# Kernel tuning notes

Hardware: AMD Instinct MI355X
Metric: run time of the kernel (lower is better)

Reference implementation:

```python
import jax, jax.numpy as jnp
import numpy as np

N_NODES = 100000
N_EDGES = 1200000
D = 64


def setup_inputs() -> dict:
    key = jax.random.key(0)
    ks = jax.random.split(key, 11)
    feats = jax.random.normal(ks[0], (N_NODES, D), dtype=jnp.float32)
    src = jax.random.randint(ks[1], (N_EDGES,), 0, N_NODES)
    dst = jax.random.randint(ks[2], (N_EDGES,), 0, N_NODES)
    s = 0.1  # small init scale
    W1 = jax.random.normal(ks[3], (D, D), dtype=jnp.float32) * s
    b1 = jnp.zeros((D,), dtype=jnp.float32)
    Wr1 = jax.random.normal(ks[4], (D, D), dtype=jnp.float32) * s
    br1 = jnp.zeros((D,), dtype=jnp.float32)
    W2 = jax.random.normal(ks[5], (D, D), dtype=jnp.float32) * s
    b2 = jnp.zeros((D,), dtype=jnp.float32)
    Wr2 = jax.random.normal(ks[6], (D, D), dtype=jnp.float32) * s
    br2 = jnp.zeros((D,), dtype=jnp.float32)
    return {"feats": feats, "W1": W1, "b1": b1, "Wr1": Wr1, "br1": br1,
            "W2": W2, "b2": b2, "Wr2": Wr2, "br2": br2,
            "src": src, "dst": dst}


def _gcn_layer(x, W, b, Wr, br, src, dst):
    # dgl GraphConv(norm='none'): aggregate sum of transformed neighbor feats + bias, then ReLU
    xw = x @ W                                        # [N, D]
    agg = jax.ops.segment_sum(xw[src], dst, num_segments=x.shape[0])  # gather-scatter
    conv = jax.nn.relu(agg + b)
    # residual branch: activation(Linear(feats))
    res = jax.nn.relu(x @ Wr + br)
    return conv + res  # dropout=0.0, batchnorm=False


def reference(feats, W1, b1, Wr1, br1, W2, b2, Wr2, br2, src, dst):
    h = _gcn_layer(feats, W1, b1, Wr1, br1, src, dst)
    h = _gcn_layer(h, W2, b2, Wr2, br2, src, dst)
    return h
```

## Files before the change

### kernel.cpp

```cpp
#include <hip/hip_runtime.h>

#define D 64
#define NBMAX 256
#define BCHUNK 4096
#define CAP 8192
#define CAP_PACK 12288

typedef unsigned short ushort_t;
typedef __attribute__((ext_vector_type(8))) short bf16x8;
typedef __attribute__((ext_vector_type(4))) float floatx4;

static __device__ __forceinline__ ushort_t f2bf(float x) {
  unsigned u = __float_as_uint(x);
  unsigned r = (u + 0x7FFF + ((u >> 16) & 1)) >> 16;
  return (ushort_t)r;
}
static __device__ __forceinline__ float bf2f(ushort_t u) {
  return __uint_as_float(((unsigned)u) << 16);
}

__global__ __launch_bounds__(256) void gemm_res_mfma_kernel(
    const float* __restrict__ x, const float* __restrict__ W,
    const float* __restrict__ Wr, const float* __restrict__ br,
    ushort_t* __restrict__ xw, ushort_t* __restrict__ res, int n_nodes,
    int* __restrict__ gtail, int* __restrict__ off_tail, int n_edges) {
  if (blockIdx.x == 0) {
    if (threadIdx.x < NBMAX) gtail[threadIdx.x] = (int)threadIdx.x * CAP_PACK;
    if (threadIdx.x == 0) *off_tail = n_edges;
  }
  const int lane = threadIdx.x & 63;
  const int wid = threadIdx.x >> 6;
  const int sub = lane & 15;
  const int q = lane >> 4;

  bf16x8 bW[4][2], bR[4][2];
#pragma unroll
  for (int t = 0; t < 4; ++t) {
#pragma unroll
    for (int s = 0; s < 2; ++s) {
      bf16x8 fw, fr;
#pragma unroll
      for (int j = 0; j < 8; ++j) {
        const int k = s * 32 + q * 8 + j;
        const int c = t * 16 + sub;
        fw[j] = (short)f2bf(W[k * D + c]);
        fr[j] = (short)f2bf(Wr[k * D + c]);
      }
      bW[t][s] = fw;
      bR[t][s] = fr;
    }
  }
  float brv[4];
#pragma unroll
  for (int t = 0; t < 4; ++t) brv[t] = br[t * 16 + sub];

  const int n_tiles = (n_nodes + 15) >> 4;
  const int wave_id = blockIdx.x * 4 + wid;
  const int n_waves = gridDim.x * 4;
  for (int tile = wave_id; tile < n_tiles; tile += n_waves) {
    const int n0 = tile << 4;
    const bool full = (n0 + 16 <= n_nodes);
    bf16x8 a0h, a0l, a1h, a1l;
    float v[16];
    if (full) {
      const float* xp = x + (size_t)(n0 + sub) * D + q * 8;
      *(float4*)(v + 0)  = *(const float4*)(xp);
      *(float4*)(v + 4)  = *(const float4*)(xp + 4);
      *(float4*)(v + 8)  = *(const float4*)(xp + 32);
      *(float4*)(v + 12) = *(const float4*)(xp + 36);
    } else {
      const bool ok = (n0 + sub) < n_nodes;
      const float* xp = x + (size_t)(n0 + sub) * D + q * 8;
#pragma unroll
      for (int j = 0; j < 8; ++j) {
        v[j] = ok ? xp[j] : 0.f;
        v[8 + j] = ok ? xp[32 + j] : 0.f;
      }
    }
#pragma unroll
    for (int j = 0; j < 8; ++j) {
      const ushort_t h0 = f2bf(v[j]);
      a0h[j] = (short)h0;
      a0l[j] = (short)f2bf(v[j] - bf2f(h0));
      const ushort_t h1 = f2bf(v[8 + j]);
      a1h[j] = (short)h1;
      a1l[j] = (short)f2bf(v[8 + j] - bf2f(h1));
    }
    floatx4 accW[4], accR[4];
#pragma unroll
    for (int t = 0; t < 4; ++t) {
      accW[t] = (floatx4){0.f, 0.f, 0.f, 0.f};
      accR[t] = (floatx4){0.f, 0.f, 0.f, 0.f};
    }
#pragma unroll
    for (int t = 0; t < 4; ++t) {
      accW[t] = __builtin_amdgcn_mfma_f32_16x16x32_bf16(a0h, bW[t][0], accW[t], 0, 0, 0);
      accW[t] = __builtin_amdgcn_mfma_f32_16x16x32_bf16(a0l, bW[t][0], accW[t], 0, 0, 0);
      accW[t] = __builtin_amdgcn_mfma_f32_16x16x32_bf16(a1h, bW[t][1], accW[t], 0, 0, 0);
      accW[t] = __builtin_amdgcn_mfma_f32_16x16x32_bf16(a1l, bW[t][1], accW[t], 0, 0, 0);
      accR[t] = __builtin_amdgcn_mfma_f32_16x16x32_bf16(a0h, bR[t][0], accR[t], 0, 0, 0);
      accR[t] = __builtin_amdgcn_mfma_f32_16x16x32_bf16(a0l, bR[t][0], accR[t], 0, 0, 0);
      accR[t] = __builtin_amdgcn_mfma_f32_16x16x32_bf16(a1h, bR[t][1], accR[t], 0, 0, 0);
      accR[t] = __builtin_amdgcn_mfma_f32_16x16x32_bf16(a1l, bR[t][1], accR[t], 0, 0, 0);
    }
    if (full) {
#pragma unroll
      for (int t = 0; t < 4; ++t) {
#pragma unroll
        for (int i = 0; i < 4; ++i) {
          const size_t r = (size_t)(n0 + q * 4 + i) * D + t * 16 + sub;
          xw[r] = f2bf(accW[t][i]);
          res[r] = f2bf(fmaxf(accR[t][i] + brv[t], 0.f));
        }
      }
    } else {
#pragma unroll
      for (int t = 0; t < 4; ++t) {
#pragma unroll
        for (int i = 0; i < 4; ++i) {
          const int rr = n0 + q * 4 + i;
          if (rr < n_nodes) {
            const size_t r = (size_t)rr * D + t * 16 + sub;
            xw[r] = f2bf(accW[t][i]);
            res[r] = f2bf(fmaxf(accR[t][i] + brv[t], 0.f));
          }
        }
      }
    }
  }
}

__global__ __launch_bounds__(256) void binpack_kernel(
    const int* __restrict__ src, const int* __restrict__ dst,
    int* __restrict__ gtail, unsigned* __restrict__ packed, int n_edges) {
  __shared__ int start[NBMAX], cur[NBMAX], gpos[NBMAX];
  __shared__ unsigned sorted[BCHUNK];
  __shared__ unsigned char bktid[BCHUNK];
  const int t = threadIdx.x;
  const int nchunk = (n_edges + BCHUNK - 1) / BCHUNK;
  for (int c = blockIdx.x; c < nchunk; c += gridDim.x) {
    cur[t] = 0;
    __syncthreads();
    const int e0 = c * BCHUNK;
    const int m = min(BCHUNK, n_edges - e0);
    int bk[16];
    unsigned pk[16];
#pragma unroll
    for (int k = 0; k < 16; ++k) {
      const int e = e0 + k * 256 + t;
      if (e < n_edges) {
        const int d = dst[e];
        const int s = src[e];
        bk[k] = d >> 9;
        pk[k] = ((unsigned)(d & 511) << 23) | (unsigned)s;
        atomicAdd(&cur[bk[k]], 1);
      } else {
        bk[k] = -1;
      }
    }
    __syncthreads();
    const int h = cur[t];
    start[t] = h;
    __syncthreads();
    for (int off = 1; off < NBMAX; off <<= 1) {
      const int v = (t >= off) ? start[t - off] : 0;
      __syncthreads();
      start[t] += v;
      __syncthreads();
    }
    const int excl = start[t] - h;
    __syncthreads();
    start[t] = excl;
    cur[t] = excl;
    __syncthreads();
#pragma unroll
    for (int k = 0; k < 16; ++k) {
      if (bk[k] >= 0) {
        const int pos = atomicAdd(&cur[bk[k]], 1);
        sorted[pos] = pk[k];
        bktid[pos] = (unsigned char)bk[k];
      }
    }
    __syncthreads();
    if (h > 0) gpos[t] = atomicAdd(&gtail[t], h);
    __syncthreads();
    for (int j = t; j < m; j += 256) {
      const int b = bktid[j];
      packed[gpos[b] + j - start[b]] = sorted[j];
    }
    __syncthreads();
  }
}

__global__ __launch_bounds__(256) void bucket_csr_kernel(
    const unsigned* __restrict__ packed, const int* __restrict__ gtail,
    int* __restrict__ csr_off, int* __restrict__ csr_src, int n_nodes,
    int nbuckets) {
  __shared__ int scnt[NBMAX], sexc[NBMAX];
  __shared__ int sc[2][512];
  __shared__ int cur[512];
  __shared__ unsigned outbuf[CAP];
  const int b = blockIdx.x;
  const int t = threadIdx.x;
  const int cb = (t < nbuckets) ? (gtail[t] - t * CAP_PACK) : 0;
  scnt[t] = cb;
  sexc[t] = cb;
  __syncthreads();
  for (int off = 1; off < NBMAX; off <<= 1) {
    const int v = (t >= off) ? sexc[t - off] : 0;
    __syncthreads();
    sexc[t] += v;
    __syncthreads();
  }
  sexc[t] -= scnt[t];
  __syncthreads();
  const int base = sexc[b];
  const int cntE = scnt[b];
  const unsigned* pk = packed + (size_t)b * CAP_PACK;

  const int n0 = b << 9;
  const int nn = min(512, n_nodes - n0);
  cur[t] = 0;
  cur[t + 256] = 0;
  __syncthreads();
  for (int i = t; i < cntE; i += 256) atomicAdd(&cur[pk[i] >> 23], 1);
  __syncthreads();
  const int h0 = cur[t];
  const int h1 = cur[t + 256];
  sc[0][t] = h0;
  sc[0][t + 256] = h1;
  __syncthreads();
  int pin = 0;
  for (int off = 1; off < 512; off <<= 1) {
    sc[1 - pin][t] = sc[pin][t] + ((t >= off) ? sc[pin][t - off] : 0);
    sc[1 - pin][t + 256] =
        sc[pin][t + 256] + ((t + 256 >= off) ? sc[pin][t + 256 - off] : 0);
    __syncthreads();
    pin ^= 1;
  }
  const int excl0 = sc[pin][t] - h0;
  const int excl1 = sc[pin][t + 256] - h1;
  if (t < nn) csr_off[n0 + t] = base + excl0;
  if (t + 256 < nn) csr_off[n0 + t + 256] = base + excl1;
  cur[t] = excl0;
  cur[t + 256] = excl1;
  __syncthreads();
  if (cntE <= CAP) {
    for (int i = t; i < cntE; i += 256) {
      const unsigned u = pk[i];
      const int pos = atomicAdd(&cur[u >> 23], 1);
      outbuf[pos] = u & 0x7FFFFFu;
    }
    __syncthreads();
    for (int j = t; j < cntE; j += 256) csr_src[base + j] = (int)outbuf[j];
  } else {
    for (int i = t; i < cntE; i += 256) {
      const unsigned u = pk[i];
      const int pos = atomicAdd(&cur[u >> 23], 1);
      csr_src[base + pos] = (int)(u & 0x7FFFFFu);
    }
  }
}

__global__ __launch_bounds__(256) void gather_gemm_kernel(
    const ushort_t* __restrict__ xw1, const ushort_t* __restrict__ res1,
    const float* __restrict__ b1v, const int* __restrict__ csr_off,
    const int* __restrict__ csr_src, const float* __restrict__ W2,
    const float* __restrict__ Wr2, const float* __restrict__ br2,
    ushort_t* __restrict__ xw2, ushort_t* __restrict__ res2, int n_nodes) {
  const int lane = threadIdx.x & 63;
  const int w = threadIdx.x >> 6;
  const int sub = lane & 15;
  const int q = lane >> 4;
  __shared__ float h_tile[16][68];

  bf16x8 bW[2], bR[2];
#pragma unroll
  for (int s = 0; s < 2; ++s) {
    bf16x8 fw, fr;
#pragma unroll
    for (int j = 0; j < 8; ++j) {
      const int k = s * 32 + q * 8 + j;
      const int c = w * 16 + sub;
      fw[j] = (short)f2bf(W2[k * D + c]);
      fr[j] = (short)f2bf(Wr2[k * D + c]);
    }
    bW[s] = fw;
    bR[s] = fr;
  }
  const float brl2 = br2[w * 16 + sub];
  const float4 bvec = *(const float4*)(b1v + sub * 4);

  const int n_tiles = (n_nodes + 15) >> 4;
  for (int tile = blockIdx.x; tile < n_tiles; tile += gridDim.x) {
    const int n0 = tile << 4;
    for (int j4 = 0; j4 < 4; ++j4) {
      const int n = n0 + w * 4 + j4;
      if (n < n_nodes) {
        const int e0 = csr_off[n];
        const int e1 = csr_off[n + 1];
        float4 acc = make_float4(0.f, 0.f, 0.f, 0.f);
        for (int base_e = e0; base_e < e1; base_e += 64) {
          const int m = min(64, e1 - base_e);
          const int idxv = (base_e + lane < e1) ? csr_src[base_e + lane] : 0;
          for (int j = 0; j < m; j += 4) {
            const int idx = __shfl(idxv, j + q, 64);
            if (j + q < m) {
              const ushort4 vv =
                  *(const ushort4*)(xw1 + ((size_t)idx << 6) + (sub << 2));
              acc.x += bf2f(vv.x);
              acc.y += bf2f(vv.y);
              acc.z += bf2f(vv.z);
              acc.w += bf2f(vv.w);
            }
          }
        }
#pragma unroll
        for (int mask = 32; mask >= 16; mask >>= 1) {
          acc.x += __shfl_xor(acc.x, mask, 64);
          acc.y += __shfl_xor(acc.y, mask, 64);
          acc.z += __shfl_xor(acc.z, mask, 64);
          acc.w += __shfl_xor(acc.w, mask, 64);
        }
        if (q == 0) {
          const ushort4 r =
              *(const ushort4*)(res1 + ((size_t)n << 6) + (sub << 2));
          float4 o;
          o.x = fmaxf(acc.x + bvec.x, 0.f) + bf2f(r.x);
          o.y = fmaxf(acc.y + bvec.y, 0.f) + bf2f(r.y);
          o.z = fmaxf(acc.z + bvec.z, 0.f) + bf2f(r.z);
          o.w = fmaxf(acc.w + bvec.w, 0.f) + bf2f(r.w);
          *(float4*)(&h_tile[w * 4 + j4][sub * 4]) = o;
        }
      } else if (q == 0) {
        *(float4*)(&h_tile[w * 4 + j4][sub * 4]) =
            make_float4(0.f, 0.f, 0.f, 0.f);
      }
    }
    __syncthreads();
    float v[16];
    *(float4*)(v + 0)  = *(const float4*)(&h_tile[sub][q * 8]);
    *(float4*)(v + 4)  = *(const float4*)(&h_tile[sub][q * 8 + 4]);
    *(float4*)(v + 8)  = *(const float4*)(&h_tile[sub][32 + q * 8]);
    *(float4*)(v + 12) = *(const float4*)(&h_tile[sub][32 + q * 8 + 4]);
    bf16x8 a0h, a0l, a1h, a1l;
#pragma unroll
    for (int j = 0; j < 8; ++j) {
      const ushort_t h0 = f2bf(v[j]);
      a0h[j] = (short)h0;
      a0l[j] = (short)f2bf(v[j] - bf2f(h0));
      const ushort_t h1 = f2bf(v[8 + j]);
      a1h[j] = (short)h1;
      a1l[j] = (short)f2bf(v[8 + j] - bf2f(h1));
    }
    floatx4 accW = (floatx4){0.f, 0.f, 0.f, 0.f};
    floatx4 accR = (floatx4){0.f, 0.f, 0.f, 0.f};
    accW = __builtin_amdgcn_mfma_f32_16x16x32_bf16(a0h, bW[0], accW, 0, 0, 0);
    accW = __builtin_amdgcn_mfma_f32_16x16x32_bf16(a0l, bW[0], accW, 0, 0, 0);
    accW = __builtin_amdgcn_mfma_f32_16x16x32_bf16(a1h, bW[1], accW, 0, 0, 0);
    accW = __builtin_amdgcn_mfma_f32_16x16x32_bf16(a1l, bW[1], accW, 0, 0, 0);
    accR = __builtin_amdgcn_mfma_f32_16x16x32_bf16(a0h, bR[0], accR, 0, 0, 0);
    accR = __builtin_amdgcn_mfma_f32_16x16x32_bf16(a0l, bR[0], accR, 0, 0, 0);
    accR = __builtin_amdgcn_mfma_f32_16x16x32_bf16(a1h, bR[1], accR, 0, 0, 0);
    accR = __builtin_amdgcn_mfma_f32_16x16x32_bf16(a1l, bR[1], accR, 0, 0, 0);
#pragma unroll
    for (int i = 0; i < 4; ++i) {
      const int rr = n0 + q * 4 + i;
      if (rr < n_nodes) {
        const size_t r = (size_t)rr * D + w * 16 + sub;
        xw2[r] = f2bf(accW[i]);
        res2[r] = f2bf(fmaxf(accR[i] + brl2, 0.f));
      }
    }
    __syncthreads();
  }
}

__global__ __launch_bounds__(256) void gather_combine_kernel(
    const ushort_t* __restrict__ xw, const ushort_t* __restrict__ res,
    const float* __restrict__ b, const int* __restrict__ csr_off,
    const int* __restrict__ csr_src, float* __restrict__ out, int n_nodes) {
  const int lane = threadIdx.x & 63;
  const int wid = threadIdx.x >> 6;
  const int grp = lane >> 4;
  const int sub = lane & 15;
  const float4 bvec = *(const float4*)(b + sub * 4);
  const int n_tiles = (n_nodes + 3) >> 2;
  for (int tile = blockIdx.x; tile < n_tiles; tile += gridDim.x) {
    const int n = tile * 4 + wid;
    if (n >= n_nodes) continue;
    const int e0 = csr_off[n];
    const int e1 = csr_off[n + 1];
    float4 acc = make_float4(0.f, 0.f, 0.f, 0.f);
    for (int base_e = e0; base_e < e1; base_e += 64) {
      const int m = min(64, e1 - base_e);
      const int idxv = (base_e + lane < e1) ? csr_src[base_e + lane] : 0;
      for (int j = 0; j < m; j += 4) {
        const int idx = __shfl(idxv, j + grp, 64);
        if (j + grp < m) {
          const ushort4 v =
              *(const ushort4*)(xw + ((size_t)idx << 6) + (sub << 2));
          acc.x += bf2f(v.x);
          acc.y += bf2f(v.y);
          acc.z += bf2f(v.z);
          acc.w += bf2f(v.w);
        }
      }
    }
#pragma unroll
    for (int mask = 32; mask >= 16; mask >>= 1) {
      acc.x += __shfl_xor(acc.x, mask, 64);
      acc.y += __shfl_xor(acc.y, mask, 64);
      acc.z += __shfl_xor(acc.z, mask, 64);
      acc.w += __shfl_xor(acc.w, mask, 64);
    }
    if (grp == 0) {
      const ushort4 r =
          *(const ushort4*)(res + ((size_t)n << 6) + (sub << 2));
      float4 o;
      o.x = fmaxf(acc.x + bvec.x, 0.f) + bf2f(r.x);
      o.y = fmaxf(acc.y + bvec.y, 0.f) + bf2f(r.y);
      o.z = fmaxf(acc.z + bvec.z, 0.f) + bf2f(r.z);
      o.w = fmaxf(acc.w + bvec.w, 0.f) + bf2f(r.w);
      *(float4*)(out + ((size_t)n << 6) + (sub << 2)) = o;
    }
  }
}

extern "C" void kernel_launch(void* const* d_in, const int* in_sizes, int n_in,
                              void* d_out, int out_size, void* d_ws, size_t ws_size,
                              hipStream_t stream) {
  const float* feats = (const float*)d_in[0];
  const float* W1  = (const float*)d_in[1];
  const float* b1  = (const float*)d_in[2];
  const float* Wr1 = (const float*)d_in[3];
  const float* br1 = (const float*)d_in[4];
  const float* W2  = (const float*)d_in[5];
  const float* b2  = (const float*)d_in[6];
  const float* Wr2 = (const float*)d_in[7];
  const float* br2 = (const float*)d_in[8];
  const int* src = (const int*)d_in[9];
  const int* dst = (const int*)d_in[10];
  const int n_nodes = in_sizes[0] / D;
  const int n_edges = in_sizes[9];
  float* out = (float*)d_out;

  const int nbuckets = (n_nodes + 511) >> 9;

  ushort_t* xw1 = (ushort_t*)d_ws;
  ushort_t* res1 = xw1 + (size_t)n_nodes * D;
  ushort_t* xw2 = res1 + (size_t)n_nodes * D;
  ushort_t* res2 = xw2 + (size_t)n_nodes * D;
  int* csr_off = (int*)(res2 + (size_t)n_nodes * D);
  int* csr_src = csr_off + (n_nodes + 1);
  int* gtail = csr_src + n_edges;
  unsigned* packed = (unsigned*)(gtail + NBMAX);

  const int tiles4 = (n_nodes + 3) / 4;
  const int gblocks = tiles4 < 2048 ? tiles4 : 2048;
  const int tiles16 = (n_nodes + 15) / 16;
  const int fblocks = tiles16 < 2048 ? tiles16 : 2048;
  const int nchunk = (n_edges + BCHUNK - 1) / BCHUNK;
  const int pblocks = nchunk < 1024 ? nchunk : 1024;
  dim3 blk(256);

  gemm_res_mfma_kernel<<<1024, blk, 0, stream>>>(
      feats, W1, Wr1, br1, xw1, res1, n_nodes, gtail, csr_off + n_nodes, n_edges);
  binpack_kernel<<<pblocks, blk, 0, stream>>>(src, dst, gtail, packed, n_edges);
  bucket_csr_kernel<<<nbuckets, blk, 0, stream>>>(packed, gtail, csr_off,
                                                  csr_src, n_nodes, nbuckets);
  gather_gemm_kernel<<<fblocks, blk, 0, stream>>>(
      xw1, res1, b1, csr_off, csr_src, W2, Wr2, br2, xw2, res2, n_nodes);
  gather_combine_kernel<<<gblocks, blk, 0, stream>>>(
      xw2, res2, b2, csr_off, csr_src, out, n_nodes);
}
```

Baseline: 252.5 us.

## Make each wave own a full 16-node tile in gather_gemm to drop block barriers

The fused gather+GEMM kernel now gives each wavefront a whole 16-node tile, with its own LDS slice and all 64 output columns, instead of splitting one tile across the four waves of a block. This removes both __syncthreads per tile, so a wave held up by high-degree nodes no longer stalls the other three. The cost is 4x more weight fragments held in registers (W2 and Wr2 for all columns) and 4x more MFMAs per wave, which raises register pressure and may lower occupancy.

```diff
diff --git a/kernel.cpp b/kernel.cpp
--- a/kernel.cpp
+++ b/kernel.cpp
@@ -272,30 +272,38 @@
   const int w = threadIdx.x >> 6;
   const int sub = lane & 15;
   const int q = lane >> 4;
-  __shared__ float h_tile[16][68];
-
-  bf16x8 bW[2], bR[2];
-#pragma unroll
-  for (int s = 0; s < 2; ++s) {
-    bf16x8 fw, fr;
-#pragma unroll
-    for (int j = 0; j < 8; ++j) {
-      const int k = s * 32 + q * 8 + j;
-      const int c = w * 16 + sub;
-      fw[j] = (short)f2bf(W2[k * D + c]);
-      fr[j] = (short)f2bf(Wr2[k * D + c]);
-    }
-    bW[s] = fw;
-    bR[s] = fr;
-  }
-  const float brl2 = br2[w * 16 + sub];
+  __shared__ float h_all[4][16][68];
+  float(*h)[68] = h_all[w];
+
+  bf16x8 bW[4][2], bR[4][2];
+#pragma unroll
+  for (int t = 0; t < 4; ++t) {
+#pragma unroll
+    for (int s = 0; s < 2; ++s) {
+      bf16x8 fw, fr;
+#pragma unroll
+      for (int j = 0; j < 8; ++j) {
+        const int k = s * 32 + q * 8 + j;
+        const int c = t * 16 + sub;
+        fw[j] = (short)f2bf(W2[k * D + c]);
+        fr[j] = (short)f2bf(Wr2[k * D + c]);
+      }
+      bW[t][s] = fw;
+      bR[t][s] = fr;
+    }
+  }
+  float brv[4];
+#pragma unroll
+  for (int t = 0; t < 4; ++t) brv[t] = br2[t * 16 + sub];
   const float4 bvec = *(const float4*)(b1v + sub * 4);
 
   const int n_tiles = (n_nodes + 15) >> 4;
-  for (int tile = blockIdx.x; tile < n_tiles; tile += gridDim.x) {
+  const int wave_id = blockIdx.x * 4 + w;
+  const int n_waves = gridDim.x * 4;
+  for (int tile = wave_id; tile < n_tiles; tile += n_waves) {
     const int n0 = tile << 4;
-    for (int j4 = 0; j4 < 4; ++j4) {
-      const int n = n0 + w * 4 + j4;
+    for (int r = 0; r < 16; ++r) {
+      const int n = n0 + r;
       if (n < n_nodes) {
         const int e0 = csr_off[n];
         const int e1 = csr_off[n + 1];
@@ -323,26 +331,24 @@
           acc.w += __shfl_xor(acc.w, mask, 64);
         }
         if (q == 0) {
-          const ushort4 r =
+          const ushort4 rr =
               *(const ushort4*)(res1 + ((size_t)n << 6) + (sub << 2));
           float4 o;
-          o.x = fmaxf(acc.x + bvec.x, 0.f) + bf2f(r.x);
-          o.y = fmaxf(acc.y + bvec.y, 0.f) + bf2f(r.y);
-          o.z = fmaxf(acc.z + bvec.z, 0.f) + bf2f(r.z);
-          o.w = fmaxf(acc.w + bvec.w, 0.f) + bf2f(r.w);
-          *(float4*)(&h_tile[w * 4 + j4][sub * 4]) = o;
+          o.x = fmaxf(acc.x + bvec.x, 0.f) + bf2f(rr.x);
+          o.y = fmaxf(acc.y + bvec.y, 0.f) + bf2f(rr.y);
+          o.z = fmaxf(acc.z + bvec.z, 0.f) + bf2f(rr.z);
+          o.w = fmaxf(acc.w + bvec.w, 0.f) + bf2f(rr.w);
+          *(float4*)(&h[r][sub * 4]) = o;
         }
       } else if (q == 0) {
-        *(float4*)(&h_tile[w * 4 + j4][sub * 4]) =
-            make_float4(0.f, 0.f, 0.f, 0.f);
-      }
-    }
-    __syncthreads();
+        *(float4*)(&h[r][sub * 4]) = make_float4(0.f, 0.f, 0.f, 0.f);
+      }
+    }
     float v[16];
-    *(float4*)(v + 0)  = *(const float4*)(&h_tile[sub][q * 8]);
-    *(float4*)(v + 4)  = *(const float4*)(&h_tile[sub][q * 8 + 4]);
-    *(float4*)(v + 8)  = *(const float4*)(&h_tile[sub][32 + q * 8]);
-    *(float4*)(v + 12) = *(const float4*)(&h_tile[sub][32 + q * 8 + 4]);
+    *(float4*)(v + 0)  = *(const float4*)(&h[sub][q * 8]);
+    *(float4*)(v + 4)  = *(const float4*)(&h[sub][q * 8 + 4]);
+    *(float4*)(v + 8)  = *(const float4*)(&h[sub][32 + q * 8]);
+    *(float4*)(v + 12) = *(const float4*)(&h[sub][32 + q * 8 + 4]);
     bf16x8 a0h, a0l, a1h, a1l;
 #pragma unroll
     for (int j = 0; j < 8; ++j) {
@@ -353,26 +359,48 @@
       a1h[j] = (short)h1;
       a1l[j] = (short)f2bf(v[8 + j] - bf2f(h1));
     }
-    floatx4 accW = (floatx4){0.f, 0.f, 0.f, 0.f};
-    floatx4 accR = (floatx4){0.f, 0.f, 0.f, 0.f};
-    accW = __builtin_amdgcn_mfma_f32_16x16x32_bf16(a0h, bW[0], accW, 0, 0, 0);
-    accW = __builtin_amdgcn_mfma_f32_16x16x32_bf16(a0l, bW[0], accW, 0, 0, 0);
-    accW = __builtin_amdgcn_mfma_f32_16x16x32_bf16(a1h, bW[1], accW, 0, 0, 0);
-    accW = __builtin_amdgcn_mfma_f32_16x16x32_bf16(a1l, bW[1], accW, 0, 0, 0);
-    accR = __builtin_amdgcn_mfma_f32_16x16x32_bf16(a0h, bR[0], accR, 0, 0, 0);
-    accR = __builtin_amdgcn_mfma_f32_16x16x32_bf16(a0l, bR[0], accR, 0, 0, 0);
-    accR = __builtin_amdgcn_mfma_f32_16x16x32_bf16(a1h, bR[1], accR, 0, 0, 0);
-    accR = __builtin_amdgcn_mfma_f32_16x16x32_bf16(a1l, bR[1], accR, 0, 0, 0);
-#pragma unroll
-    for (int i = 0; i < 4; ++i) {
-      const int rr = n0 + q * 4 + i;
-      if (rr < n_nodes) {
-        const size_t r = (size_t)rr * D + w * 16 + sub;
-        xw2[r] = f2bf(accW[i]);
-        res2[r] = f2bf(fmaxf(accR[i] + brl2, 0.f));
-      }
-    }
-    __syncthreads();
+    floatx4 accW[4], accR[4];
+#pragma unroll
+    for (int t = 0; t < 4; ++t) {
+      accW[t] = (floatx4){0.f, 0.f, 0.f, 0.f};
+      accR[t] = (floatx4){0.f, 0.f, 0.f, 0.f};
+    }
+#pragma unroll
+    for (int t = 0; t < 4; ++t) {
+      accW[t] = __builtin_amdgcn_mfma_f32_16x16x32_bf16(a0h, bW[t][0], accW[t], 0, 0, 0);
+      accW[t] = __builtin_amdgcn_mfma_f32_16x16x32_bf16(a0l, bW[t][0], accW[t], 0, 0, 0);
+      accW[t] = __builtin_amdgcn_mfma_f32_16x16x32_bf16(a1h, bW[t][1], accW[t], 0, 0, 0);
+      accW[t] = __builtin_amdgcn_mfma_f32_16x16x32_bf16(a1l, bW[t][1], accW[t], 0, 0, 0);
+      accR[t] = __builtin_amdgcn_mfma_f32_16x16x32_bf16(a0h, bR[t][0], accR[t], 0, 0, 0);
+      accR[t] = __builtin_amdgcn_mfma_f32_16x16x32_bf16(a0l, bR[t][0], accR[t], 0, 0, 0);
+      accR[t] = __builtin_amdgcn_mfma_f32_16x16x32_bf16(a1h, bR[t][1], accR[t], 0, 0, 0);
+      accR[t] = __builtin_amdgcn_mfma_f32_16x16x32_bf16(a1l, bR[t][1], accR[t], 0, 0, 0);
+    }
+    const bool full = (n0 + 16 <= n_nodes);
+    if (full) {
+#pragma unroll
+      for (int t = 0; t < 4; ++t) {
+#pragma unroll
+        for (int i = 0; i < 4; ++i) {
+          const size_t r = (size_t)(n0 + q * 4 + i) * D + t * 16 + sub;
+          xw2[r] = f2bf(accW[t][i]);
+          res2[r] = f2bf(fmaxf(accR[t][i] + brv[t], 0.f));
+        }
+      }
+    } else {
+#pragma unroll
+      for (int t = 0; t < 4; ++t) {
+#pragma unroll
+        for (int i = 0; i < 4; ++i) {
+          const int rr = n0 + q * 4 + i;
+          if (rr < n_nodes) {
+            const size_t r = (size_t)rr * D + t * 16 + sub;
+            xw2[r] = f2bf(accW[t][i]);
+            res2[r] = f2bf(fmaxf(accR[t][i] + brv[t], 0.f));
+          }
+        }
+      }
+    }
   }
 }
 
```

Result: slower. 299.7 us (+18.7%).
